# Kernel tuning notes

Hardware: AMD Instinct MI355X
Metric: run time of the kernel (lower is better)

Reference implementation:

```python
import jax, jax.numpy as jnp
import numpy as np

B, HID, NH = 2048, 512, 8
HD = HID // NH


def _slstm(x, W, b, R, h, c):
    # gates = W_gates(x) + R_gates(h); chunk order i,f,g,o
    g = x @ W.T + b + h @ R.T
    i, f, gg, o = jnp.split(g, 4, axis=1)
    c_new = jax.nn.sigmoid(f) * c + jnp.exp(i) * jnp.tanh(gg)
    return jax.nn.sigmoid(o) * jnp.tanh(c_new)


def _mlstm(x, Wq, bq, Wk, bk, Wv, bv, igw, igb, fgw, fgb, lng, lnb):
    Bsz = x.shape[0]
    q = (x @ Wq.T + bq).reshape(Bsz, NH, HD)
    k = (x @ Wk.T + bk).reshape(Bsz, NH, HD)
    v = (x @ Wv.T + bv).reshape(Bsz, NH, HD)
    i = jnp.exp(x @ igw.T + igb)            # [B,H] input gate (exponential)
    f = jax.nn.sigmoid(x @ fgw.T + fgb)     # [B,H]; multiplies zero init state -> drops out
    # initial state (C, n, m) is zeros, so C_new = i * (v k^T), n_new = i * v, m_new = i
    C = i[:, :, None, None] * (v[..., :, None] * k[..., None, :])  # [B,H,hd,hd]
    n = i[:, :, None] * v                                          # [B,H,hd]
    m = i                                                          # [B,H]
    num = jnp.einsum('bhij,bhj->bhi', C, q)
    den = jnp.einsum('bhi,bhi->bh', n, q) + m + 1e-6
    h = (num / den[..., None]).reshape(Bsz, HID)
    mu = h.mean(-1, keepdims=True)
    var = ((h - mu) ** 2).mean(-1, keepdims=True)
    return (h - mu) / jnp.sqrt(var + 1e-5) * lng + lnb


def setup_inputs() -> dict:
    key = jax.random.key(0)
    ks = iter(jax.random.split(key, 64))
    rn = lambda shape, s: jax.random.normal(next(ks), shape, dtype=jnp.float32) * s
    inp = {
        'V': jax.random.normal(next(ks), (B, 1), dtype=jnp.float32),
        't': jax.random.uniform(next(ks), (B, 1), dtype=jnp.float32),
        'ip_w': rn((HID, 2), 0.1), 'ip_b': rn((HID,), 0.02),
        'op_w': rn((1, HID), 0.05), 'op_b': rn((1,), 0.02),
    }
    for p in ('s0', 's2'):
        inp[p + '_W'] = rn((4 * HID, HID), 0.05)
        inp[p + '_b'] = rn((4 * HID,), 0.05)
        inp[p + '_R'] = rn((4 * HID, HID), 0.05)
    for p in ('m1', 'm3'):
        for nm in ('Wq', 'Wk', 'Wv'):
            inp[p + '_' + nm] = rn((HID, HID), 0.05)
        for nm in ('bq', 'bk', 'bv'):
            inp[p + '_' + nm] = rn((HID,), 0.02)
        inp[p + '_igw'] = rn((NH, HID), 0.05)
        inp[p + '_igb'] = rn((NH,), 0.1)
        inp[p + '_fgw'] = rn((NH, HID), 0.05)
        inp[p + '_fgb'] = jnp.linspace(3.0, 6.0, NH, dtype=jnp.float32)
        inp[p + '_lng'] = jnp.ones((HID,), dtype=jnp.float32)
        inp[p + '_lnb'] = jnp.zeros((HID,), dtype=jnp.float32)
    return inp


def reference(V, t, ip_w, ip_b, op_w, op_b,
              s0_W, s0_b, s0_R, s2_W, s2_b, s2_R,
              m1_Wq, m1_Wk, m1_Wv, m1_bq, m1_bk, m1_bv,
              m1_igw, m1_igb, m1_fgw, m1_fgb, m1_lng, m1_lnb,
              m3_Wq, m3_Wk, m3_Wv, m3_bq, m3_bk, m3_bv,
              m3_igw, m3_igb, m3_fgw, m3_fgb, m3_lng, m3_lnb):
    x = jnp.concatenate([V, t], axis=1)           # [B,2]
    h = x @ ip_w.T + ip_b                         # [B,HID]
    z = jnp.zeros((h.shape[0], HID), h.dtype)
    h = _slstm(h, s0_W, s0_b, s0_R, z, z)         # layer 0: sLSTM
    h = _mlstm(h, m1_Wq, m1_bq, m1_Wk, m1_bk, m1_Wv, m1_bv,
               m1_igw, m1_igb, m1_fgw, m1_fgb, m1_lng, m1_lnb)  # layer 1: mLSTM
    h = _slstm(h, s2_W, s2_b, s2_R, z, z)         # layer 2: sLSTM
    h = _mlstm(h, m3_Wq, m3_bq, m3_Wk, m3_bk, m3_Wv, m3_bv,
               m3_igw, m3_igb, m3_fgw, m3_fgb, m3_lng, m3_lnb)  # layer 3: mLSTM
    return h @ op_w.T + op_b                      # I_pred [B,1]
```

## Files before the change

### kernel.cpp

```cpp
#include <hip/hip_runtime.h>
#include <hip/hip_bf16.h>

#define HID 512
#define BATCH 2048

typedef __bf16 bf16x8 __attribute__((ext_vector_type(8)));
typedef float f32x4 __attribute__((ext_vector_type(4)));
typedef float f32x16 __attribute__((ext_vector_type(16)));
typedef __hip_bfloat16 bf16;

__device__ inline unsigned short f2bf(float x) {
    bf16 h = __float2bfloat16(x);
    return __builtin_bit_cast(unsigned short, h);
}
__device__ inline float bf2f(unsigned short u) {
    return __bfloat162float(__builtin_bit_cast(bf16, u));
}

__device__ inline void gload16(const void* g, void* l) {
    __builtin_amdgcn_global_load_lds((const __attribute__((address_space(1))) void*)g,
                                     (__attribute__((address_space(3))) void*)l, 16, 0, 0);
}

struct CvtArgs { const float* src[8]; };

__global__ void k_prep(CvtArgs a, unsigned short* __restrict__ hi, unsigned short* __restrict__ lo,
                       const float* __restrict__ V, const float* __restrict__ t,
                       const float* __restrict__ ipw, const float* __restrict__ ipb,
                       unsigned short* __restrict__ hhi, unsigned short* __restrict__ hlo) {
    const int bid = blockIdx.x;
    if (bid < 3584) {
        int idx4 = (bid * 256 + threadIdx.x) << 2;
        int seg, off;
        if (idx4 < 2097152) { seg = idx4 >> 20; off = idx4 & 1048575; }
        else { int r = idx4 - 2097152; seg = 2 + (r >> 18); off = r & 262143; }
        f32x4 w = *(const f32x4*)(a.src[seg] + off);
        ushort4 h, l;
        h.x = f2bf(w[0]); h.y = f2bf(w[1]); h.z = f2bf(w[2]); h.w = f2bf(w[3]);
        l.x = f2bf(w[0] - bf2f(h.x)); l.y = f2bf(w[1] - bf2f(h.y));
        l.z = f2bf(w[2] - bf2f(h.z)); l.w = f2bf(w[3] - bf2f(h.w));
        *(ushort4*)(hi + idx4) = h;
        *(ushort4*)(lo + idx4) = l;
    } else {
        int idx = (bid - 3584) * 256 + threadIdx.x;
        int b = idx >> 7, j4 = (idx & 127) << 2;
        float vv = V[b], tt = t[b];
        f32x4 w0 = *(const f32x4*)(ipw + 2 * j4);
        f32x4 w1 = *(const f32x4*)(ipw + 2 * j4 + 4);
        f32x4 bb = *(const f32x4*)(ipb + j4);
        float x[4] = { w0[0] * vv + w0[1] * tt + bb[0], w0[2] * vv + w0[3] * tt + bb[1],
                       w1[0] * vv + w1[1] * tt + bb[2], w1[2] * vv + w1[3] * tt + bb[3] };
        ushort4 h, l;
        h.x = f2bf(x[0]); h.y = f2bf(x[1]); h.z = f2bf(x[2]); h.w = f2bf(x[3]);
        l.x = f2bf(x[0] - bf2f(h.x)); l.y = f2bf(x[1] - bf2f(h.y));
        l.z = f2bf(x[2] - bf2f(h.z)); l.w = f2bf(x[3] - bf2f(h.w));
        size_t o = (size_t)b * HID + j4;
        *(ushort4*)(hhi + o) = h;
        *(ushort4*)(hlo + o) = l;
    }
}

__global__ __launch_bounds__(256, 2) void k_gemm(
    const bf16* __restrict__ Ahi, const bf16* __restrict__ Alo,
    const bf16* __restrict__ Wh0, const bf16* __restrict__ Wh1, const bf16* __restrict__ Wh2,
    const bf16* __restrict__ Wl0, const bf16* __restrict__ Wl1, const bf16* __restrict__ Wl2,
    float* __restrict__ C)
{
    __shared__ __align__(16) bf16 lds[3][8192];
    const int tid = threadIdx.x, w = tid >> 6, lane = tid & 63;

    const int bid = blockIdx.x;
    const int xcd = bid & 7, slot = bid >> 3;
    const int m0 = (xcd * 2 + slot / 12) * 128;
    const int n0 = (slot % 12) * 128;
    const int nseg = n0 >> 9, nloc = n0 & 511;
    const bf16* Wh = nseg == 0 ? Wh0 : (nseg == 1 ? Wh1 : Wh2);
    const bf16* Wl = nseg == 0 ? Wl0 : (nseg == 1 ? Wl1 : Wl2);

    const bf16* msrc = (w == 0) ? Ahi : (w == 1) ? Alo : (w == 2) ? Wh : Wl;
    const int rowbase = (w < 2) ? m0 : nloc;
    const size_t srow = (size_t)(rowbase + (lane & 31)) * HID + ((lane >> 5) << 3);

    auto STAGE = [&](int t) {
        bf16* db = &lds[t % 3][0] + (w << 11) + (lane << 3);
        const bf16* gp = msrc + srow + (t << 4);
#pragma unroll
        for (int p = 0; p < 4; ++p)
            gload16(gp + (size_t)(p << 5) * HID, db + (p << 9));
    };

    const int wm = w >> 1, wn = w & 1;
    const int la = lane << 3;
    f32x16 acc00 = {}, acc01 = {}, acc10 = {}, acc11 = {};

    STAGE(0);
    STAGE(1);
    for (int t = 0; t < 32; ++t) {
        if (t < 31)
            asm volatile("s_waitcnt vmcnt(4) lgkmcnt(0)\n\ts_barrier" ::: "memory");
        else
            asm volatile("s_waitcnt vmcnt(0) lgkmcnt(0)\n\ts_barrier" ::: "memory");
        if (t < 30) STAGE(t + 2);
        const bf16* lb = &lds[t % 3][0];
        bf16x8 ah0 = *(const bf16x8*)(lb + ((2 * wm    ) << 9) + la);
        bf16x8 ah1 = *(const bf16x8*)(lb + ((2 * wm + 1) << 9) + la);
        bf16x8 al0 = *(const bf16x8*)(lb + ((4 + 2 * wm    ) << 9) + la);
        bf16x8 al1 = *(const bf16x8*)(lb + ((4 + 2 * wm + 1) << 9) + la);
        bf16x8 wh0 = *(const bf16x8*)(lb + ((8 + 2 * wn    ) << 9) + la);
        bf16x8 wh1 = *(const bf16x8*)(lb + ((8 + 2 * wn + 1) << 9) + la);
        bf16x8 wl0 = *(const bf16x8*)(lb + ((12 + 2 * wn    ) << 9) + la);
        bf16x8 wl1 = *(const bf16x8*)(lb + ((12 + 2 * wn + 1) << 9) + la);
        acc00 = __builtin_amdgcn_mfma_f32_32x32x16_bf16(ah0, wh0, acc00, 0, 0, 0);
        acc01 = __builtin_amdgcn_mfma_f32_32x32x16_bf16(ah0, wh1, acc01, 0, 0, 0);
        acc10 = __builtin_amdgcn_mfma_f32_32x32x16_bf16(ah1, wh0, acc10, 0, 0, 0);
        acc11 = __builtin_amdgcn_mfma_f32_32x32x16_bf16(ah1, wh1, acc11, 0, 0, 0);
        acc00 = __builtin_amdgcn_mfma_f32_32x32x16_bf16(al0, wh0, acc00, 0, 0, 0);
        acc01 = __builtin_amdgcn_mfma_f32_32x32x16_bf16(al0, wh1, acc01, 0, 0, 0);
        acc10 = __builtin_amdgcn_mfma_f32_32x32x16_bf16(al1, wh0, acc10, 0, 0, 0);
        acc11 = __builtin_amdgcn_mfma_f32_32x32x16_bf16(al1, wh1, acc11, 0, 0, 0);
        acc00 = __builtin_amdgcn_mfma_f32_32x32x16_bf16(ah0, wl0, acc00, 0, 0, 0);
        acc01 = __builtin_amdgcn_mfma_f32_32x32x16_bf16(ah0, wl1, acc01, 0, 0, 0);
        acc10 = __builtin_amdgcn_mfma_f32_32x32x16_bf16(ah1, wl0, acc10, 0, 0, 0);
        acc11 = __builtin_amdgcn_mfma_f32_32x32x16_bf16(ah1, wl1, acc11, 0, 0, 0);
    }

    const f32x16* accs[2][2] = { { &acc00, &acc01 }, { &acc10, &acc11 } };
#pragma unroll
    for (int fi = 0; fi < 2; ++fi)
#pragma unroll
        for (int fj = 0; fj < 2; ++fj) {
            const f32x16& ac = *accs[fi][fj];
            const int col = n0 + ((2 * wn + fj) << 5) + (lane & 31);
            const int rbase = m0 + ((2 * wm + fi) << 5) + ((lane >> 5) << 2);
#pragma unroll
            for (int rr = 0; rr < 16; ++rr) {
                int row = rbase + (rr & 3) + ((rr >> 2) << 3);
                C[(size_t)row * 1536 + col] = ac[rr];
            }
        }
}

__global__ void k_slstm_act(const float* __restrict__ g, const float* __restrict__ bp,
                            unsigned short* __restrict__ hhi, unsigned short* __restrict__ hlo) {
    int idx = blockIdx.x * blockDim.x + threadIdx.x;
    int b = idx >> 7, j4 = (idx & 127) << 2;
    const float* r0 = g + (size_t)b * 1536 + j4;
    f32x4 gi = *(const f32x4*)r0 + *(const f32x4*)(bp + j4);
    f32x4 gg = *(const f32x4*)(r0 + 512) + *(const f32x4*)(bp + 1024 + j4);
    f32x4 go = *(const f32x4*)(r0 + 1024) + *(const f32x4*)(bp + 1536 + j4);
    ushort4 h, l;
    float x[4];
#pragma unroll
    for (int u = 0; u < 4; ++u)
        x[u] = tanhf(expf(gi[u]) * tanhf(gg[u])) / (1.f + expf(-go[u]));
    h.x = f2bf(x[0]); h.y = f2bf(x[1]); h.z = f2bf(x[2]); h.w = f2bf(x[3]);
    l.x = f2bf(x[0] - bf2f(h.x)); l.y = f2bf(x[1] - bf2f(h.y));
    l.z = f2bf(x[2] - bf2f(h.z)); l.w = f2bf(x[3] - bf2f(h.w));
    size_t o = (size_t)b * HID + j4;
    *(ushort4*)(hhi + o) = h;
    *(ushort4*)(hlo + o) = l;
}

__global__ __launch_bounds__(512) void k_mlstm(
    const float* __restrict__ g0,
    const float* __restrict__ bq, const float* __restrict__ bk, const float* __restrict__ bv,
    const bf16* __restrict__ hinh, const bf16* __restrict__ hinl,
    const float* __restrict__ igw, const float* __restrict__ igb,
    const float* __restrict__ lng, const float* __restrict__ lnb,
    unsigned short* __restrict__ outh, unsigned short* __restrict__ outl,
    const float* __restrict__ opw, const float* __restrict__ opb, float* __restrict__ out)
{
    int b = blockIdx.x;
    int tid = threadIdx.x, head = tid >> 6, lane = tid & 63;

    const bf16*  hh = hinh + (size_t)b * HID;
    const bf16*  hl = hinl + (size_t)b * HID;
    const float* wrow = igw + head * HID;
    float s = 0.f;
#pragma unroll
    for (int k = 0; k < 8; ++k) {
        int p = lane + 64 * k;
        s += wrow[p] * (__bfloat162float(hh[p]) + __bfloat162float(hl[p]));
    }
#pragma unroll
    for (int off = 32; off; off >>= 1) s += __shfl_xor(s, off);
    float ig = expf(s + igb[head]);

    const float* r0 = g0 + (size_t)b * 1536;
    float q  = r0[tid] + bq[tid];
    float kk = r0[512 + tid] + bk[tid];
    float v  = r0[1024 + tid] + bv[tid];
    float kq = kk * q, vq = v * q;
#pragma unroll
    for (int off = 32; off; off >>= 1) { kq += __shfl_xor(kq, off); vq += __shfl_xor(vq, off); }
    float den = ig * (vq + 1.0f) + 1e-6f;
    float hv  = v * (ig * kq) / den;

    __shared__ float red[16];
    __shared__ float red2[8];
    float s1 = hv, s2 = hv * hv;
#pragma unroll
    for (int off = 32; off; off >>= 1) { s1 += __shfl_xor(s1, off); s2 += __shfl_xor(s2, off); }
    if (lane == 0) { red[head] = s1; red[8 + head] = s2; }
    __syncthreads();
    float t1 = 0.f, t2 = 0.f;
#pragma unroll
    for (int h2 = 0; h2 < 8; ++h2) { t1 += red[h2]; t2 += red[8 + h2]; }
    float mu  = t1 * (1.f / 512.f);
    float var = t2 * (1.f / 512.f) - mu * mu;
    float o = (hv - mu) * rsqrtf(var + 1e-5f) * lng[tid] + lnb[tid];

    if (out) {
        float po = o * opw[tid];
#pragma unroll
        for (int off = 32; off; off >>= 1) po += __shfl_xor(po, off);
        if (lane == 0) red2[head] = po;
        __syncthreads();
        if (tid == 0) {
            float tt = 0.f;
#pragma unroll
            for (int h2 = 0; h2 < 8; ++h2) tt += red2[h2];
            out[b] = tt + opb[0];
        }
    } else {
        unsigned short oh = f2bf(o);
        size_t p = (size_t)b * HID + tid;
        outh[p] = oh;
        outl[p] = f2bf(o - bf2f(oh));
    }
}

extern "C" void kernel_launch(void* const* d_in, const int* in_sizes, int n_in,
                              void* d_out, int out_size, void* d_ws, size_t ws_size,
                              hipStream_t stream) {
    const float* V    = (const float*)d_in[0];
    const float* t    = (const float*)d_in[1];
    const float* ip_w = (const float*)d_in[2];
    const float* ip_b = (const float*)d_in[3];
    const float* op_w = (const float*)d_in[4];
    const float* op_b = (const float*)d_in[5];
    const float* s0_W = (const float*)d_in[6];
    const float* s0_b = (const float*)d_in[7];
    const float* s2_W = (const float*)d_in[9];
    const float* s2_b = (const float*)d_in[10];
    const float* m1_Wq = (const float*)d_in[12];
    const float* m1_Wk = (const float*)d_in[13];
    const float* m1_Wv = (const float*)d_in[14];
    const float* m1_bq = (const float*)d_in[15];
    const float* m1_bk = (const float*)d_in[16];
    const float* m1_bv = (const float*)d_in[17];
    const float* m1_igw = (const float*)d_in[18];
    const float* m1_igb = (const float*)d_in[19];
    const float* m1_lng = (const float*)d_in[22];
    const float* m1_lnb = (const float*)d_in[23];
    const float* m3_Wq = (const float*)d_in[24];
    const float* m3_Wk = (const float*)d_in[25];
    const float* m3_Wv = (const float*)d_in[26];
    const float* m3_bq = (const float*)d_in[27];
    const float* m3_bk = (const float*)d_in[28];
    const float* m3_bv = (const float*)d_in[29];
    const float* m3_igw = (const float*)d_in[30];
    const float* m3_igb = (const float*)d_in[31];
    const float* m3_lng = (const float*)d_in[34];
    const float* m3_lnb = (const float*)d_in[35];

    char* ws = (char*)d_ws;
    bf16* whi  = (bf16*)ws;
    bf16* wlo  = (bf16*)(ws + 7340032);
    bf16* hAhi = (bf16*)(ws + 14680064);
    bf16* hAlo = (bf16*)(ws + 16777216);
    bf16* hBhi = (bf16*)(ws + 18874368);
    bf16* hBlo = (bf16*)(ws + 20971520);
    float* gq0 = (float*)(ws + 23068672);

    CvtArgs ca;
    ca.src[0] = s0_W; ca.src[1] = s2_W;
    ca.src[2] = m1_Wq; ca.src[3] = m1_Wk; ca.src[4] = m1_Wv;
    ca.src[5] = m3_Wq; ca.src[6] = m3_Wk; ca.src[7] = m3_Wv;
    k_prep<<<4608, 256, 0, stream>>>(ca, (unsigned short*)whi, (unsigned short*)wlo,
                                     V, t, ip_w, ip_b,
                                     (unsigned short*)hAhi, (unsigned short*)hAlo);

    k_gemm<<<192, 256, 0, stream>>>(hAhi, hAlo,
        whi + 0, whi + 524288, whi + 786432,
        wlo + 0, wlo + 524288, wlo + 786432, gq0);
    k_slstm_act<<<1024, 256, 0, stream>>>(gq0, s0_b, (unsigned short*)hBhi, (unsigned short*)hBlo);
    k_gemm<<<192, 256, 0, stream>>>(hBhi, hBlo,
        whi + 2097152, whi + 2359296, whi + 2621440,
        wlo + 2097152, wlo + 2359296, wlo + 2621440, gq0);
    k_mlstm<<<BATCH, 512, 0, stream>>>(gq0, m1_bq, m1_bk, m1_bv, hBhi, hBlo,
                                       m1_igw, m1_igb, m1_lng, m1_lnb,
                                       (unsigned short*)hAhi, (unsigned short*)hAlo,
                                       nullptr, nullptr, nullptr);
    k_gemm<<<192, 256, 0, stream>>>(hAhi, hAlo,
        whi + 1048576, whi + 1572864, whi + 1835008,
        wlo + 1048576, wlo + 1572864, wlo + 1835008, gq0);
    k_slstm_act<<<1024, 256, 0, stream>>>(gq0, s2_b, (unsigned short*)hBhi, (unsigned short*)hBlo);
    k_gemm<<<192, 256, 0, stream>>>(hBhi, hBlo,
        whi + 2883584, whi + 3145728, whi + 3407872,
        wlo + 2883584, wlo + 3145728, wlo + 3407872, gq0);
    k_mlstm<<<BATCH, 512, 0, stream>>>(gq0, m3_bq, m3_bk, m3_bv, hBhi, hBlo,
                                       m3_igw, m3_igb, m3_lng, m3_lnb,
                                       nullptr, nullptr,
                                       op_w, op_b, (float*)d_out);
}
```

Measured before the change: 122.0 us.

## Fold rank-2 input projection into first sLSTM weights, drop first GEMM

The input projection is rank 2 (V, t), so the first sLSTM gates are linear in V and t. The change precomputes W_s0·ip_w columns and W_s0·ip_b + b_s0 for the i, g and o gates with a per-row wave reduction. It then evaluates the first layer elementwise in a new kernel, which removes a full 2048x1536x512 split-bf16 GEMM and the conversion of s0_W to bf16. The first layer is now computed in fp32 rather than hi/lo bf16, which may shift numerics slightly.

Result: faster. 101.2 us (-17.1%).

```diff
diff --git a/kernel.cpp b/kernel.cpp
--- a/kernel.cpp
+++ b/kernel.cpp
@@ -22,42 +22,70 @@
                                      (__attribute__((address_space(3))) void*)l, 16, 0, 0);
 }
 
-struct CvtArgs { const float* src[8]; };
+struct CvtArgs { const float* src[7]; };
 
 __global__ void k_prep(CvtArgs a, unsigned short* __restrict__ hi, unsigned short* __restrict__ lo,
-                       const float* __restrict__ V, const float* __restrict__ t,
+                       const float* __restrict__ s0W, const float* __restrict__ s0b,
                        const float* __restrict__ ipw, const float* __restrict__ ipb,
-                       unsigned short* __restrict__ hhi, unsigned short* __restrict__ hlo) {
+                       float* __restrict__ uV, float* __restrict__ uT, float* __restrict__ uC) {
     const int bid = blockIdx.x;
-    if (bid < 3584) {
+    if (bid < 2560) {
         int idx4 = (bid * 256 + threadIdx.x) << 2;
-        int seg, off;
-        if (idx4 < 2097152) { seg = idx4 >> 20; off = idx4 & 1048575; }
-        else { int r = idx4 - 2097152; seg = 2 + (r >> 18); off = r & 262143; }
+        int seg, off; size_t dst;
+        if (idx4 < 1048576) { seg = 0; off = idx4; dst = 1048576 + idx4; }
+        else { int r = idx4 - 1048576; seg = 1 + (r >> 18); off = r & 262143; dst = 2097152 + r; }
         f32x4 w = *(const f32x4*)(a.src[seg] + off);
         ushort4 h, l;
         h.x = f2bf(w[0]); h.y = f2bf(w[1]); h.z = f2bf(w[2]); h.w = f2bf(w[3]);
         l.x = f2bf(w[0] - bf2f(h.x)); l.y = f2bf(w[1] - bf2f(h.y));
         l.z = f2bf(w[2] - bf2f(h.z)); l.w = f2bf(w[3] - bf2f(h.w));
-        *(ushort4*)(hi + idx4) = h;
-        *(ushort4*)(lo + idx4) = l;
+        *(ushort4*)(hi + dst) = h;
+        *(ushort4*)(lo + dst) = l;
     } else {
-        int idx = (bid - 3584) * 256 + threadIdx.x;
-        int b = idx >> 7, j4 = (idx & 127) << 2;
-        float vv = V[b], tt = t[b];
-        f32x4 w0 = *(const f32x4*)(ipw + 2 * j4);
-        f32x4 w1 = *(const f32x4*)(ipw + 2 * j4 + 4);
-        f32x4 bb = *(const f32x4*)(ipb + j4);
-        float x[4] = { w0[0] * vv + w0[1] * tt + bb[0], w0[2] * vv + w0[3] * tt + bb[1],
-                       w1[0] * vv + w1[1] * tt + bb[2], w1[2] * vv + w1[3] * tt + bb[3] };
-        ushort4 h, l;
-        h.x = f2bf(x[0]); h.y = f2bf(x[1]); h.z = f2bf(x[2]); h.w = f2bf(x[3]);
-        l.x = f2bf(x[0] - bf2f(h.x)); l.y = f2bf(x[1] - bf2f(h.y));
-        l.z = f2bf(x[2] - bf2f(h.z)); l.w = f2bf(x[3] - bf2f(h.w));
-        size_t o = (size_t)b * HID + j4;
-        *(ushort4*)(hhi + o) = h;
-        *(ushort4*)(hlo + o) = l;
+        const int w = threadIdx.x >> 6, lane = threadIdx.x & 63;
+        const int r = (bid - 2560) * 4 + w;
+        const int wr = r < 512 ? r : r + 512;
+        const float* Wp = s0W + (size_t)wr * HID + lane * 8;
+        f32x4 wa = *(const f32x4*)Wp, wb = *(const f32x4*)(Wp + 4);
+        const float* pw = ipw + lane * 16;
+        f32x4 e0 = *(const f32x4*)pw,       e1 = *(const f32x4*)(pw + 4);
+        f32x4 e2 = *(const f32x4*)(pw + 8), e3 = *(const f32x4*)(pw + 12);
+        f32x4 ba = *(const f32x4*)(ipb + lane * 8), bb = *(const f32x4*)(ipb + lane * 8 + 4);
+        float s0 = wa[0]*e0[0] + wa[1]*e0[2] + wa[2]*e1[0] + wa[3]*e1[2]
+                 + wb[0]*e2[0] + wb[1]*e2[2] + wb[2]*e3[0] + wb[3]*e3[2];
+        float s1 = wa[0]*e0[1] + wa[1]*e0[3] + wa[2]*e1[1] + wa[3]*e1[3]
+                 + wb[0]*e2[1] + wb[1]*e2[3] + wb[2]*e3[1] + wb[3]*e3[3];
+        float s2 = wa[0]*ba[0] + wa[1]*ba[1] + wa[2]*ba[2] + wa[3]*ba[3]
+                 + wb[0]*bb[0] + wb[1]*bb[1] + wb[2]*bb[2] + wb[3]*bb[3];
+#pragma unroll
+        for (int off = 32; off; off >>= 1) {
+            s0 += __shfl_xor(s0, off); s1 += __shfl_xor(s1, off); s2 += __shfl_xor(s2, off);
+        }
+        if (lane == 0) { uV[r] = s0; uT[r] = s1; uC[r] = s2 + s0b[wr]; }
     }
+}
+
+__global__ void k_slstm0(const float* __restrict__ V, const float* __restrict__ t,
+                         const float* __restrict__ uV, const float* __restrict__ uT,
+                         const float* __restrict__ uC,
+                         unsigned short* __restrict__ hhi, unsigned short* __restrict__ hlo) {
+    int idx = blockIdx.x * blockDim.x + threadIdx.x;
+    int b = idx >> 7, j4 = (idx & 127) << 2;
+    float vv = V[b], tt = t[b];
+    f32x4 gi = vv * *(const f32x4*)(uV + j4)        + tt * *(const f32x4*)(uT + j4)        + *(const f32x4*)(uC + j4);
+    f32x4 gg = vv * *(const f32x4*)(uV + 512 + j4)  + tt * *(const f32x4*)(uT + 512 + j4)  + *(const f32x4*)(uC + 512 + j4);
+    f32x4 go = vv * *(const f32x4*)(uV + 1024 + j4) + tt * *(const f32x4*)(uT + 1024 + j4) + *(const f32x4*)(uC + 1024 + j4);
+    ushort4 h, l;
+    float x[4];
+#pragma unroll
+    for (int u = 0; u < 4; ++u)
+        x[u] = tanhf(expf(gi[u]) * tanhf(gg[u])) / (1.f + expf(-go[u]));
+    h.x = f2bf(x[0]); h.y = f2bf(x[1]); h.z = f2bf(x[2]); h.w = f2bf(x[3]);
+    l.x = f2bf(x[0] - bf2f(h.x)); l.y = f2bf(x[1] - bf2f(h.y));
+    l.z = f2bf(x[2] - bf2f(h.z)); l.w = f2bf(x[3] - bf2f(h.w));
+    size_t o = (size_t)b * HID + j4;
+    *(ushort4*)(hhi + o) = h;
+    *(ushort4*)(hlo + o) = l;
 }
 
 __global__ __launch_bounds__(256, 2) void k_gemm(
@@ -271,35 +299,35 @@
     bf16* hAlo = (bf16*)(ws + 16777216);
     bf16* hBhi = (bf16*)(ws + 18874368);
     bf16* hBlo = (bf16*)(ws + 20971520);
-    float* gq0 = (float*)(ws + 23068672);
+    float* gq  = (float*)(ws + 23068672);
+    float* uV  = (float*)(ws + 35651584);
+    float* uT  = uV + 1536;
+    float* uC  = uT + 1536;
 
     CvtArgs ca;
-    ca.src[0] = s0_W; ca.src[1] = s2_W;
-    ca.src[2] = m1_Wq; ca.src[3] = m1_Wk; ca.src[4] = m1_Wv;
-    ca.src[5] = m3_Wq; ca.src[6] = m3_Wk; ca.src[7] = m3_Wv;
-    k_prep<<<4608, 256, 0, stream>>>(ca, (unsigned short*)whi, (unsigned short*)wlo,
-                                     V, t, ip_w, ip_b,
-                                     (unsigned short*)hAhi, (unsigned short*)hAlo);
-
-    k_gemm<<<192, 256, 0, stream>>>(hAhi, hAlo,
-        whi + 0, whi + 524288, whi + 786432,
-        wlo + 0, wlo + 524288, wlo + 786432, gq0);
-    k_slstm_act<<<1024, 256, 0, stream>>>(gq0, s0_b, (unsigned short*)hBhi, (unsigned short*)hBlo);
+    ca.src[0] = s2_W;
+    ca.src[1] = m1_Wq; ca.src[2] = m1_Wk; ca.src[3] = m1_Wv;
+    ca.src[4] = m3_Wq; ca.src[5] = m3_Wk; ca.src[6] = m3_Wv;
+    k_prep<<<2944, 256, 0, stream>>>(ca, (unsigned short*)whi, (unsigned short*)wlo,
+                                     s0_W, s0_b, ip_w, ip_b, uV, uT, uC);
+
+    k_slstm0<<<1024, 256, 0, stream>>>(V, t, uV, uT, uC,
+                                       (unsigned short*)hBhi, (unsigned short*)hBlo);
     k_gemm<<<192, 256, 0, stream>>>(hBhi, hBlo,
         whi + 2097152, whi + 2359296, whi + 2621440,
-        wlo + 2097152, wlo + 2359296, wlo + 2621440, gq0);
-    k_mlstm<<<BATCH, 512, 0, stream>>>(gq0, m1_bq, m1_bk, m1_bv, hBhi, hBlo,
+        wlo + 2097152, wlo + 2359296, wlo + 2621440, gq);
+    k_mlstm<<<BATCH, 512, 0, stream>>>(gq, m1_bq, m1_bk, m1_bv, hBhi, hBlo,
                                        m1_igw, m1_igb, m1_lng, m1_lnb,
                                        (unsigned short*)hAhi, (unsigned short*)hAlo,
                                        nullptr, nullptr, nullptr);
     k_gemm<<<192, 256, 0, stream>>>(hAhi, hAlo,
         whi + 1048576, whi + 1572864, whi + 1835008,
-        wlo + 1048576, wlo + 1572864, wlo + 1835008, gq0);
-    k_slstm_act<<<1024, 256, 0, stream>>>(gq0, s2_b, (unsigned short*)hBhi, (unsigned short*)hBlo);
+        wlo + 1048576, wlo + 1572864, wlo + 1835008, gq);
+    k_slstm_act<<<1024, 256, 0, stream>>>(gq, s2_b, (unsigned short*)hBhi, (unsigned short*)hBlo);
     k_gemm<<<192, 256, 0, stream>>>(hBhi, hBlo,
         whi + 2883584, whi + 3145728, whi + 3407872,
-        wlo + 2883584, wlo + 3145728, wlo + 3407872, gq0);
-    k_mlstm<<<BATCH, 512, 0, stream>>>(gq0, m3_bq, m3_bk, m3_bv, hBhi, hBlo,
+        wlo + 2883584, wlo + 3145728, wlo + 3407872, gq);
+    k_mlstm<<<BATCH, 512, 0, stream>>>(gq, m3_bq, m3_bk, m3_bv, hBhi, hBlo,
                                        m3_igw, m3_igb, m3_lng, m3_lnb,
                                        nullptr, nullptr,
                                        op_w, op_b, (float*)d_out);
```
